# Optimization experiments

Hardware: AMD Instinct MI355X
Metric: run time of the kernel (lower is better)

Reference implementation:

```python
import jax, jax.numpy as jnp
import numpy as np

DELTA_BEARING = 30.0
DELTA_HEADING = 30.0
N_HEAD = int(360 / DELTA_HEADING)  # 12
N_BEAR = int(360 / DELTA_BEARING)  # 12
B, P, D = 512, 128, 64
EPS = 1e-5


def setup_inputs() -> dict:
    key = jax.random.key(0)
    ks = jax.random.split(key, 8)
    hidden_state = jax.random.normal(ks[0], (B, P, D), dtype=jnp.float32)
    distance_matrix = jax.random.uniform(ks[1], (B, P, P), dtype=jnp.float32) * 10.0
    bearing_matrix = jax.random.uniform(ks[2], (B, P, P), dtype=jnp.float32) * 360.0
    heading_matrix = jax.random.uniform(ks[3], (B, P, P), dtype=jnp.float32) * 360.0
    sequence_mask = (jax.random.uniform(ks[4], (B, P)) < 0.8).astype(jnp.float32)
    domain = jax.random.normal(ks[5], (N_HEAD, N_BEAR), dtype=jnp.float32) * 2.0 + 5.0
    W = jax.random.normal(ks[6], (D, 2 * D), dtype=jnp.float32) / np.sqrt(2 * D)
    b = jnp.zeros((D,), dtype=jnp.float32)
    return {"hidden_state": hidden_state, "distance_matrix": distance_matrix,
            "bearing_matrix": bearing_matrix, "heading_matrix": heading_matrix,
            "sequence_mask": sequence_mask, "domain": domain, "W": W, "b": b}


def reference(hidden_state, distance_matrix, bearing_matrix, heading_matrix,
              sequence_mask, domain, W, b):
    # discretized relative-pose lookup indices
    idx1 = jnp.clip(jnp.floor(heading_matrix / DELTA_HEADING), 0, N_HEAD - 1).astype(jnp.int32)
    idx2 = jnp.clip(jnp.floor(bearing_matrix / DELTA_BEARING), 0, N_BEAR - 1).astype(jnp.int32)
    # gather from learned domain table, subtract distance, relu  -> [B,P,P]
    w = jax.nn.relu(domain[idx1, idx2] - distance_matrix)
    # zero the diagonal (self-interaction) and invalid pedestrian pairs
    eye = jnp.eye(P, dtype=bool)
    pair_mask = sequence_mask[:, :, None] * sequence_mask[:, None, :]  # [B,P,P]
    w = jnp.where(eye[None, :, :], 0.0, w)
    w = jnp.where(pair_mask != 0, w, 0.0)
    # masked softmax over dim=2: mask = (w != 0)
    mask = (w != 0).astype(w.dtype)
    masked_exps = jnp.exp(w) * mask + EPS
    weights = masked_exps / (masked_exps.sum(axis=2, keepdims=True) + EPS)
    # aggregate neighbor hidden states and fuse
    weighted_hidden = jnp.einsum('bpq,bqd->bpd', weights, hidden_state)
    fused = jnp.concatenate([weighted_hidden, hidden_state], axis=2)  # [B,P,2D]
    out = jnp.tanh(fused @ W.T + b)
    return out
```

## Files before the change

### kernel.cpp

```cpp
#include <hip/hip_runtime.h>
#include <hip/hip_bf16.h>
#include <math.h>

#define NB 512
#define NP 128
#define ND 64
#define EPSF 1e-5f
#define SW 136

typedef __attribute__((ext_vector_type(8))) short short8;
typedef __attribute__((ext_vector_type(4))) float f32x4;

__device__ __forceinline__ short f2bf(float x) {
    __hip_bfloat16 h = __float2bfloat16(x);
    return *reinterpret_cast<short*>(&h);
}

__global__ __launch_bounds__(512, 4) void spatial_attn_kernel(
    const float* __restrict__ hidden,
    const float* __restrict__ dist,
    const float* __restrict__ bear,
    const float* __restrict__ head,
    const float* __restrict__ smask,
    const float* __restrict__ domain,
    const float* __restrict__ W,
    const float* __restrict__ bias,
    float* __restrict__ out)
{
    __shared__ __align__(16) short s_w[NP * SW];
    __shared__ __align__(16) short s_hT[ND * SW];
    __shared__ __align__(16) short s_Wm[ND * SW];
    __shared__ float s_dom[144];
    __shared__ float s_mask[NP];

    const int b    = blockIdx.x;
    const int tid  = threadIdx.x;
    const int lane = tid & 63;
    const int wave = tid >> 6;
    const int quad = lane >> 4;
    const int l16  = lane & 15;

    {
        const float4* hsrc = (const float4*)(hidden + (size_t)b * NP * ND);
        #pragma unroll
        for (int i = 0; i < 4; ++i) {
            int idx = tid + i * 512;
            float4 v = hsrc[idx];
            int q = idx >> 4;
            int d = (idx & 15) * 4;
            s_hT[(d + 0) * SW + q] = f2bf(v.x);
            s_hT[(d + 1) * SW + q] = f2bf(v.y);
            s_hT[(d + 2) * SW + q] = f2bf(v.z);
            s_hT[(d + 3) * SW + q] = f2bf(v.w);
        }
    }
    {
        #pragma unroll
        for (int i = 0; i < 4; ++i) {
            int idx = tid + i * 512;
            float4 v = ((const float4*)W)[idx];
            int d = idx >> 5;
            int k = (idx & 31) * 4;
            short4 s4;
            s4.x = f2bf(v.x); s4.y = f2bf(v.y); s4.z = f2bf(v.z); s4.w = f2bf(v.w);
            *(short4*)&s_Wm[d * SW + k] = s4;
        }
    }
    if (tid < 144) s_dom[tid] = domain[tid];
    if (tid < NP)  s_mask[tid] = smask[b * NP + tid];
    __syncthreads();

    const int R0 = wave * 16;
    const size_t rowbase = (size_t)b * NP * NP;
    const float mq0 = s_mask[lane], mq1 = s_mask[lane + 64];

    for (int j0 = 0; j0 < 16; j0 += 4) {
        #pragma unroll
        for (int r = 0; r < 4; ++r) {
            const int p = R0 + j0 + r;
            const size_t ro = rowbase + (size_t)p * NP;
            float dq0 = dist[ro + lane], dq1 = dist[ro + lane + 64];
            float bq0 = bear[ro + lane], bq1 = bear[ro + lane + 64];
            float hq0 = head[ro + lane], hq1 = head[ro + lane + 64];
            const float mp = s_mask[p];

            int i1 = (int)floorf(hq0 / 30.0f); i1 = i1 < 0 ? 0 : (i1 > 11 ? 11 : i1);
            int i2 = (int)floorf(bq0 / 30.0f); i2 = i2 < 0 ? 0 : (i2 > 11 ? 11 : i2);
            float wv0 = s_dom[i1 * 12 + i2] - dq0;
            bool on0 = (wv0 > 0.0f) && (mp != 0.0f) && (mq0 != 0.0f) && (lane != p);
            float e0 = on0 ? (expf(wv0) + EPSF) : EPSF;

            int k1 = (int)floorf(hq1 / 30.0f); k1 = k1 < 0 ? 0 : (k1 > 11 ? 11 : k1);
            int k2 = (int)floorf(bq1 / 30.0f); k2 = k2 < 0 ? 0 : (k2 > 11 ? 11 : k2);
            float wv1 = s_dom[k1 * 12 + k2] - dq1;
            bool on1 = (wv1 > 0.0f) && (mp != 0.0f) && (mq1 != 0.0f) && ((lane + 64) != p);
            float e1 = on1 ? (expf(wv1) + EPSF) : EPSF;

            s_w[p * SW + lane]      = f2bf(e0);
            s_w[p * SW + lane + 64] = f2bf(e1);
        }
    }

    f32x4 acc[4], accs;
    #pragma unroll
    for (int tj = 0; tj < 4; ++tj) acc[tj] = (f32x4){0.f, 0.f, 0.f, 0.f};
    accs = (f32x4){0.f, 0.f, 0.f, 0.f};

    short8 ones;
    #pragma unroll
    for (int i = 0; i < 8; ++i) ones[i] = (short)0x3F80;

    #pragma unroll
    for (int kb = 0; kb < 4; ++kb) {
        const int ko = kb * 32 + quad * 8;
        short8 a = *(const short8*)&s_w[(R0 + l16) * SW + ko];
        accs = __builtin_amdgcn_mfma_f32_16x16x32_bf16(a, ones, accs, 0, 0, 0);
        #pragma unroll
        for (int tj = 0; tj < 4; ++tj) {
            short8 bf = *(const short8*)&s_hT[(tj * 16 + l16) * SW + ko];
            acc[tj] = __builtin_amdgcn_mfma_f32_16x16x32_bf16(a, bf, acc[tj], 0, 0, 0);
        }
    }

    float inv[4];
    #pragma unroll
    for (int r = 0; r < 4; ++r) inv[r] = 1.0f / (accs[r] + EPSF);

    #pragma unroll
    for (int tj = 0; tj < 4; ++tj)
        #pragma unroll
        for (int r = 0; r < 4; ++r) {
            int row = R0 + quad * 4 + r;
            s_w[row * SW + tj * 16 + l16] = f2bf(acc[tj][r] * inv[r]);
        }
    {
        const float* hb = hidden + (size_t)b * NP * ND;
        #pragma unroll 4
        for (int i = 0; i < 16; ++i) {
            float hv = hb[(size_t)(R0 + i) * ND + lane];
            s_w[(R0 + i) * SW + 64 + lane] = f2bf(hv);
        }
    }

    f32x4 acc2[4];
    #pragma unroll
    for (int tj = 0; tj < 4; ++tj) acc2[tj] = (f32x4){0.f, 0.f, 0.f, 0.f};

    #pragma unroll
    for (int kb = 0; kb < 4; ++kb) {
        const int ko = kb * 32 + quad * 8;
        short8 a = *(const short8*)&s_w[(R0 + l16) * SW + ko];
        #pragma unroll
        for (int tj = 0; tj < 4; ++tj) {
            short8 bf = *(const short8*)&s_Wm[(tj * 16 + l16) * SW + ko];
            acc2[tj] = __builtin_amdgcn_mfma_f32_16x16x32_bf16(a, bf, acc2[tj], 0, 0, 0);
        }
    }

    float bvals[4];
    #pragma unroll
    for (int tj = 0; tj < 4; ++tj) bvals[tj] = bias[tj * 16 + l16];

    float* ob = out + (size_t)b * NP * ND;
    #pragma unroll
    for (int tj = 0; tj < 4; ++tj)
        #pragma unroll
        for (int r = 0; r < 4; ++r) {
            int row = R0 + quad * 4 + r;
            ob[(size_t)row * ND + tj * 16 + l16] = tanhf(acc2[tj][r] + bvals[tj]);
        }
}

extern "C" void kernel_launch(void* const* d_in, const int* in_sizes, int n_in,
                              void* d_out, int out_size, void* d_ws, size_t ws_size,
                              hipStream_t stream) {
    const float* hidden = (const float*)d_in[0];
    const float* dist   = (const float*)d_in[1];
    const float* bear   = (const float*)d_in[2];
    const float* head   = (const float*)d_in[3];
    const float* smask  = (const float*)d_in[4];
    const float* domain = (const float*)d_in[5];
    const float* W      = (const float*)d_in[6];
    const float* bias   = (const float*)d_in[7];
    float* out = (float*)d_out;

    spatial_attn_kernel<<<dim3(NB), dim3(512), 0, stream>>>(
        hidden, dist, bear, head, smask, domain, W, bias, out);
}
```

Measured before the change: 157.2 us.

## Split each batch across two blocks, pre-convert W to bf16, use fast math

Each batch is now handled by two 256-thread blocks, one per half of the query rows. This doubles the grid and cuts per-block LDS so more blocks can be resident per CU. W is converted to bf16 once by a small prep kernel into a global buffer, and the second GEMM reads it directly instead of every block converting it into LDS. The exp and tanh calls become fast intrinsics, and the angle binning uses a multiply by 1/30 in double. The cost is that each block still loads and transposes the full hidden tensor for its batch, so that load is now done twice per batch, plus an extra kernel launch.

```diff
diff --git a/kernel.cpp b/kernel.cpp
--- a/kernel.cpp
+++ b/kernel.cpp
@@ -16,24 +16,45 @@
     return *reinterpret_cast<short*>(&h);
 }
 
-__global__ __launch_bounds__(512, 4) void spatial_attn_kernel(
+__device__ __forceinline__ int bin30(float x) {
+    float t = (float)((double)x * (1.0 / 30.0));
+    int i = (int)t;
+    return i < 0 ? 0 : (i > 11 ? 11 : i);
+}
+
+__device__ __forceinline__ float fast_tanh(float x) {
+    float e = __expf(2.0f * x);
+    return 1.0f - 2.0f * __builtin_amdgcn_rcpf(e + 1.0f);
+}
+
+__device__ __align__(16) short g_wbf[ND * 2 * ND];
+
+__global__ __launch_bounds__(256) void prep_w(const float* __restrict__ W) {
+    int idx = blockIdx.x * 256 + threadIdx.x;
+    float4 v = ((const float4*)W)[idx];
+    short4 s4;
+    s4.x = f2bf(v.x); s4.y = f2bf(v.y); s4.z = f2bf(v.z); s4.w = f2bf(v.w);
+    *(short4*)&g_wbf[idx * 4] = s4;
+}
+
+__global__ __launch_bounds__(256, 4) void spatial_attn_kernel(
     const float* __restrict__ hidden,
     const float* __restrict__ dist,
     const float* __restrict__ bear,
     const float* __restrict__ head,
     const float* __restrict__ smask,
     const float* __restrict__ domain,
-    const float* __restrict__ W,
     const float* __restrict__ bias,
     float* __restrict__ out)
 {
-    __shared__ __align__(16) short s_w[NP * SW];
+    __shared__ __align__(16) short s_w[64 * SW];
     __shared__ __align__(16) short s_hT[ND * SW];
-    __shared__ __align__(16) short s_Wm[ND * SW];
     __shared__ float s_dom[144];
     __shared__ float s_mask[NP];
 
-    const int b    = blockIdx.x;
+    const int blk  = blockIdx.x;
+    const int b    = blk >> 1;
+    const int half = blk & 1;
     const int tid  = threadIdx.x;
     const int lane = tid & 63;
     const int wave = tid >> 6;
@@ -43,8 +64,8 @@
     {
         const float4* hsrc = (const float4*)(hidden + (size_t)b * NP * ND);
         #pragma unroll
-        for (int i = 0; i < 4; ++i) {
-            int idx = tid + i * 512;
+        for (int i = 0; i < 8; ++i) {
+            int idx = i * 256 + ((tid & 15) * 16 + (tid >> 4));
             float4 v = hsrc[idx];
             int q = idx >> 4;
             int d = (idx & 15) * 4;
@@ -54,50 +75,38 @@
             s_hT[(d + 3) * SW + q] = f2bf(v.w);
         }
     }
-    {
-        #pragma unroll
-        for (int i = 0; i < 4; ++i) {
-            int idx = tid + i * 512;
-            float4 v = ((const float4*)W)[idx];
-            int d = idx >> 5;
-            int k = (idx & 31) * 4;
-            short4 s4;
-            s4.x = f2bf(v.x); s4.y = f2bf(v.y); s4.z = f2bf(v.z); s4.w = f2bf(v.w);
-            *(short4*)&s_Wm[d * SW + k] = s4;
-        }
-    }
     if (tid < 144) s_dom[tid] = domain[tid];
     if (tid < NP)  s_mask[tid] = smask[b * NP + tid];
     __syncthreads();
 
-    const int R0 = wave * 16;
+    const int R0L = wave * 16;
+    const int P0  = half * 64 + R0L;
     const size_t rowbase = (size_t)b * NP * NP;
     const float mq0 = s_mask[lane], mq1 = s_mask[lane + 64];
 
     for (int j0 = 0; j0 < 16; j0 += 4) {
         #pragma unroll
         for (int r = 0; r < 4; ++r) {
-            const int p = R0 + j0 + r;
+            const int p = P0 + j0 + r;
+            const int rl = R0L + j0 + r;
             const size_t ro = rowbase + (size_t)p * NP;
             float dq0 = dist[ro + lane], dq1 = dist[ro + lane + 64];
             float bq0 = bear[ro + lane], bq1 = bear[ro + lane + 64];
             float hq0 = head[ro + lane], hq1 = head[ro + lane + 64];
             const float mp = s_mask[p];
 
-            int i1 = (int)floorf(hq0 / 30.0f); i1 = i1 < 0 ? 0 : (i1 > 11 ? 11 : i1);
-            int i2 = (int)floorf(bq0 / 30.0f); i2 = i2 < 0 ? 0 : (i2 > 11 ? 11 : i2);
+            int i1 = bin30(hq0), i2 = bin30(bq0);
             float wv0 = s_dom[i1 * 12 + i2] - dq0;
             bool on0 = (wv0 > 0.0f) && (mp != 0.0f) && (mq0 != 0.0f) && (lane != p);
-            float e0 = on0 ? (expf(wv0) + EPSF) : EPSF;
+            float e0 = on0 ? (__expf(wv0) + EPSF) : EPSF;
 
-            int k1 = (int)floorf(hq1 / 30.0f); k1 = k1 < 0 ? 0 : (k1 > 11 ? 11 : k1);
-            int k2 = (int)floorf(bq1 / 30.0f); k2 = k2 < 0 ? 0 : (k2 > 11 ? 11 : k2);
+            int k1 = bin30(hq1), k2 = bin30(bq1);
             float wv1 = s_dom[k1 * 12 + k2] - dq1;
             bool on1 = (wv1 > 0.0f) && (mp != 0.0f) && (mq1 != 0.0f) && ((lane + 64) != p);
-            float e1 = on1 ? (expf(wv1) + EPSF) : EPSF;
+            float e1 = on1 ? (__expf(wv1) + EPSF) : EPSF;
 
-            s_w[p * SW + lane]      = f2bf(e0);
-            s_w[p * SW + lane + 64] = f2bf(e1);
+            s_w[rl * SW + lane]      = f2bf(e0);
+            s_w[rl * SW + lane + 64] = f2bf(e1);
         }
     }
 
@@ -113,7 +122,7 @@
     #pragma unroll
     for (int kb = 0; kb < 4; ++kb) {
         const int ko = kb * 32 + quad * 8;
-        short8 a = *(const short8*)&s_w[(R0 + l16) * SW + ko];
+        short8 a = *(const short8*)&s_w[(R0L + l16) * SW + ko];
         accs = __builtin_amdgcn_mfma_f32_16x16x32_bf16(a, ones, accs, 0, 0, 0);
         #pragma unroll
         for (int tj = 0; tj < 4; ++tj) {
@@ -130,15 +139,15 @@
     for (int tj = 0; tj < 4; ++tj)
         #pragma unroll
         for (int r = 0; r < 4; ++r) {
-            int row = R0 + quad * 4 + r;
+            int row = R0L + quad * 4 + r;
             s_w[row * SW + tj * 16 + l16] = f2bf(acc[tj][r] * inv[r]);
         }
     {
-        const float* hb = hidden + (size_t)b * NP * ND;
+        const float* hb = hidden + ((size_t)b * NP + P0 - R0L) * ND;
         #pragma unroll 4
         for (int i = 0; i < 16; ++i) {
-            float hv = hb[(size_t)(R0 + i) * ND + lane];
-            s_w[(R0 + i) * SW + 64 + lane] = f2bf(hv);
+            float hv = hb[(size_t)(R0L + i) * ND + lane];
+            s_w[(R0L + i) * SW + 64 + lane] = f2bf(hv);
         }
     }
 
@@ -149,10 +158,10 @@
     #pragma unroll
     for (int kb = 0; kb < 4; ++kb) {
         const int ko = kb * 32 + quad * 8;
-        short8 a = *(const short8*)&s_w[(R0 + l16) * SW + ko];
+        short8 a = *(const short8*)&s_w[(R0L + l16) * SW + ko];
         #pragma unroll
         for (int tj = 0; tj < 4; ++tj) {
-            short8 bf = *(const short8*)&s_Wm[(tj * 16 + l16) * SW + ko];
+            short8 bf = *(const short8*)&g_wbf[(tj * 16 + l16) * (2 * ND) + ko];
             acc2[tj] = __builtin_amdgcn_mfma_f32_16x16x32_bf16(a, bf, acc2[tj], 0, 0, 0);
         }
     }
@@ -161,13 +170,13 @@
     #pragma unroll
     for (int tj = 0; tj < 4; ++tj) bvals[tj] = bias[tj * 16 + l16];
 
-    float* ob = out + (size_t)b * NP * ND;
+    float* ob = out + ((size_t)b * NP + half * 64) * ND;
     #pragma unroll
     for (int tj = 0; tj < 4; ++tj)
         #pragma unroll
         for (int r = 0; r < 4; ++r) {
-            int row = R0 + quad * 4 + r;
-            ob[(size_t)row * ND + tj * 16 + l16] = tanhf(acc2[tj][r] + bvals[tj]);
+            int row = R0L + quad * 4 + r;
+            ob[(size_t)row * ND + tj * 16 + l16] = fast_tanh(acc2[tj][r] + bvals[tj]);
         }
 }
 
@@ -184,6 +193,7 @@
     const float* bias   = (const float*)d_in[7];
     float* out = (float*)d_out;
 
-    spatial_attn_kernel<<<dim3(NB), dim3(512), 0, stream>>>(
-        hidden, dist, bear, head, smask, domain, W, bias, out);
+    prep_w<<<dim3(8), dim3(256), 0, stream>>>(W);
+    spatial_attn_kernel<<<dim3(NB * 2), dim3(256), 0, stream>>>(
+        hidden, dist, bear, head, smask, domain, bias, out);
 }
```

Result: no change. 158.5 us (+0.8%).
